# Kernel optimization log

Hardware: AMD Instinct MI355X
Metric: run time of the kernel (lower is better)

Reference implementation:

```python
import jax, jax.numpy as jnp
import numpy as np

NUM_HEADS = 16
WINDOW = 256  # window_size; tokens attend iff |i-j| <= WINDOW//2
LN_EPS = 1e-5


def setup_inputs() -> dict:
    key = jax.random.key(0)
    k1, k2, k3 = jax.random.split(key, 3)
    B, L, D = 2, 2048, 1024
    x = jax.random.normal(k1, (B, L, D), dtype=jnp.float32)
    w_qkv = jax.random.normal(k2, (3 * D, D), dtype=jnp.float32) * 0.02
    w_out = jax.random.normal(k3, (D, D), dtype=jnp.float32) * 0.02
    gamma = jnp.ones((D,), dtype=jnp.float32)
    beta = jnp.zeros((D,), dtype=jnp.float32)
    return {"x": x, "w_qkv": w_qkv, "w_out": w_out, "gamma": gamma, "beta": beta}


def reference(x, w_qkv, w_out, gamma, beta):
    B, L, D = x.shape
    H = NUM_HEADS
    HD = D // H
    residual = x
    # LayerNorm
    mu = jnp.mean(x, axis=-1, keepdims=True)
    var = jnp.mean(jnp.square(x - mu), axis=-1, keepdims=True)
    xn = (x - mu) * jax.lax.rsqrt(var + LN_EPS) * gamma + beta
    # QKV projection (torch Linear: y = x @ W.T)
    qkv = jnp.einsum('bld,ed->ble', xn, w_qkv).reshape(B, L, 3, H, HD)
    qkv = jnp.transpose(qkv, (2, 0, 3, 1, 4))  # [3, B, H, L, HD]
    q, k, v = qkv[0], qkv[1], qkv[2]
    # Dense scores with banded window mask (same math as the torch module)
    scores = jnp.einsum('bhqd,bhkd->bhqk', q, k) / jnp.sqrt(jnp.float32(HD))
    idx = jnp.arange(L)
    band = jnp.abs(idx[:, None] - idx[None, :]) <= (WINDOW // 2)  # [L, L] bool
    scores = jnp.where(band[None, None], scores, -jnp.inf)
    attn = jax.nn.softmax(scores, axis=-1)
    out = jnp.einsum('bhqk,bhkd->bhqd', attn, v)  # [B, H, L, HD]
    out = jnp.transpose(out, (0, 2, 1, 3)).reshape(B, L, D)
    return residual + jnp.einsum('bld,ed->ble', out, w_out)
```

## Files before the change

kernel.cpp:

```cpp
#include <hip/hip_runtime.h>

typedef unsigned int u32;
typedef unsigned short u16;
typedef __attribute__((ext_vector_type(8))) short short8;
typedef __attribute__((ext_vector_type(4))) float f32x4;

#define LSEQ 2048
#define DM 1024
#define HWIN 128
#define QSCALE 0.1803368801111204f

__device__ __forceinline__ u32 pk(float lo, float hi) {
  u32 r;
  asm("v_cvt_pk_bf16_f32 %0, %1, %2" : "=v"(r) : "v"(lo), "v"(hi));
  return r;
}
__device__ __forceinline__ u16 f2bf(float f) {
  union { float f; u32 u; } v; v.f = f;
  u32 r = v.u + 0x7FFFu + ((v.u >> 16) & 1u);
  return (u16)(r >> 16);
}
__device__ __forceinline__ u32 packbf(float lo, float hi) {
  return (u32)f2bf(lo) | ((u32)f2bf(hi) << 16);
}

typedef __attribute__((address_space(3))) u32 lds_u32;
typedef __attribute__((address_space(1))) const u32 glob_u32;
__device__ __forceinline__ void g2lds16(const void* g, void* l) {
  __builtin_amdgcn_global_load_lds((glob_u32*)g, (lds_u32*)l, 16, 0, 0);
}

__global__ __launch_bounds__(256) void ln_cvt_kernel(const float* __restrict__ x,
                                                     const float* __restrict__ gamma,
                                                     const float* __restrict__ beta,
                                                     u16* __restrict__ xn,
                                                     const float* __restrict__ wqi,
                                                     const float* __restrict__ woi,
                                                     u16* __restrict__ wq,
                                                     u16* __restrict__ wo) {
  int blk = blockIdx.x;
  int t = threadIdx.x;
  if (blk >= 4096) {
    const float* in; u16* out; int i;
    if (blk < 7168) { in = wqi; out = wq; i = (blk - 4096) * 256 + t; }
    else            { in = woi; out = wo; i = (blk - 7168) * 256 + t; }
    float4 v = ((const float4*)in)[i];
    u32* dst = (u32*)out + i * 2;
    dst[0] = pk(v.x, v.y);
    dst[1] = pk(v.z, v.w);
    return;
  }
  int r = blk;
  const float4* xr = (const float4*)(x + (size_t)r * DM);
  float4 v = xr[t];
  float s = v.x + v.y + v.z + v.w;
  float s2 = v.x * v.x + v.y * v.y + v.z * v.z + v.w * v.w;
#pragma unroll
  for (int o = 32; o; o >>= 1) { s += __shfl_xor(s, o); s2 += __shfl_xor(s2, o); }
  __shared__ float ws1[4], ws2[4];
  if ((t & 63) == 0) { ws1[t >> 6] = s; ws2[t >> 6] = s2; }
  __syncthreads();
  s = ws1[0] + ws1[1] + ws1[2] + ws1[3];
  s2 = ws2[0] + ws2[1] + ws2[2] + ws2[3];
  float mu = s * (1.0f / DM);
  float var = s2 * (1.0f / DM) - mu * mu;
  float rs = rsqrtf(var + 1e-5f);
  float4 g = ((const float4*)gamma)[t];
  float4 b = ((const float4*)beta)[t];
  u32* dst = (u32*)(xn + (size_t)r * DM) + t * 2;
  dst[0] = pk((v.x - mu) * rs * g.x + b.x, (v.y - mu) * rs * g.y + b.y);
  dst[1] = pk((v.z - mu) * rs * g.z + b.z, (v.w - mu) * rs * g.w + b.w);
}

__device__ __forceinline__ void stage_tile(const u16* __restrict__ G, int gr0, int K,
                                           int k0, u16* lbuf, int tid, int w) {
#pragma unroll
  for (int j = 0; j < 4; ++j) {
    int rp = j * 32 + (tid >> 3);
    int ce = ((tid & 7) ^ (rp & 7)) * 8;
    g2lds16(G + (size_t)(gr0 + rp) * K + k0 + ce, lbuf + j * 2048 + w * 512);
  }
}

template <int MODE>
__global__ __launch_bounds__(256) void gemm_bt(const u16* __restrict__ Ag,
                                               const u16* __restrict__ Bg,
                                               int K, int NB, int NT,
                                               u16* __restrict__ qk_out,
                                               u16* __restrict__ vt_out,
                                               const float* __restrict__ resid,
                                               float* __restrict__ out) {
  __shared__ __align__(16) u16 sm[32768];
  int tid = threadIdx.x;
  int w = tid >> 6, l = tid & 63;
  int lg = l >> 4, li = l & 15;
  int wr = w >> 1, wc = w & 1;

  for (int tile = blockIdx.x; tile < NT; tile += gridDim.x) {
    int bm = tile / NB, bn = tile % NB;
    f32x4 acc[4][4];
#pragma unroll
    for (int m = 0; m < 4; ++m)
#pragma unroll
      for (int n = 0; n < 4; ++n) acc[m][n] = (f32x4){0.f, 0.f, 0.f, 0.f};

    int nt = K >> 6;
    stage_tile(Ag, bm * 128, K, 0, sm, tid, w);
    stage_tile(Bg, bn * 128, K, 0, sm + 8192, tid, w);
    asm volatile("s_waitcnt vmcnt(0)" ::: "memory");
    __builtin_amdgcn_s_barrier();
    asm volatile("" ::: "memory");

    int cur = 0;
    for (int t = 0; t < nt; ++t) {
      if (t + 1 < nt) {
        stage_tile(Ag, bm * 128, K, (t + 1) << 6, sm + (cur ^ 1) * 16384, tid, w);
        stage_tile(Bg, bn * 128, K, (t + 1) << 6, sm + (cur ^ 1) * 16384 + 8192, tid, w);
      }
      const u16* Ab = sm + cur * 16384;
      const u16* Bb = Ab + 8192;
#pragma unroll
      for (int ks = 0; ks < 2; ++ks) {
        short8 af[4], bf4[4];
#pragma unroll
        for (int m = 0; m < 4; ++m)
          af[m] = *(const short8*)&Ab[(wr * 64 + m * 16 + li) * 64 + (((lg + ks * 4) ^ (li & 7)) * 8)];
#pragma unroll
        for (int n = 0; n < 4; ++n)
          bf4[n] = *(const short8*)&Bb[(wc * 64 + n * 16 + li) * 64 + (((lg + ks * 4) ^ (li & 7)) * 8)];
#pragma unroll
        for (int m = 0; m < 4; ++m)
#pragma unroll
          for (int n = 0; n < 4; ++n)
            acc[m][n] = __builtin_amdgcn_mfma_f32_16x16x32_bf16(af[m], bf4[n], acc[m][n], 0, 0, 0);
      }
      asm volatile("s_waitcnt vmcnt(0)" ::: "memory");
      __builtin_amdgcn_s_barrier();
      asm volatile("" ::: "memory");
      cur ^= 1;
    }

    int colbase = bn * 128 + wc * 64;
    int rowbase = bm * 128 + wr * 64;
#pragma unroll
    for (int m = 0; m < 4; ++m) {
      int row = rowbase + m * 16 + lg * 4;
#pragma unroll
      for (int n = 0; n < 4; ++n) {
        int col = colbase + n * 16 + li;
        if (MODE == 0) {
          if (colbase < 2048) {
            float qs = (colbase < 1024) ? QSCALE : 1.0f;
            u32 p01 = pk(acc[m][n][0] * qs, acc[m][n][1] * qs);
            u32 p23 = pk(acc[m][n][2] * qs, acc[m][n][3] * qs);
            qk_out[(size_t)(row + 0) * 2048 + col] = (u16)p01;
            qk_out[(size_t)(row + 1) * 2048 + col] = (u16)(p01 >> 16);
            qk_out[(size_t)(row + 2) * 2048 + col] = (u16)p23;
            qk_out[(size_t)(row + 3) * 2048 + col] = (u16)(p23 >> 16);
          } else {
            int b = row >> 11;
            int hdcol = col - 2048;
            size_t idx = ((size_t)b * 1024 + hdcol) * 2048 + (row & 2047);
            u32* d = (u32*)&vt_out[idx];
            d[0] = pk(acc[m][n][0], acc[m][n][1]);
            d[1] = pk(acc[m][n][2], acc[m][n][3]);
          }
        } else {
#pragma unroll
          for (int r = 0; r < 4; ++r) {
            size_t idx = (size_t)(row + r) * 1024 + col;
            out[idx] = resid[idx] + acc[m][n][r];
          }
        }
      }
    }
  }
}

__global__ __launch_bounds__(256) void attn_kernel(const u16* __restrict__ qk,
                                                   const u16* __restrict__ vt,
                                                   u16* __restrict__ ato) {
  int blk0 = blockIdx.x;
  int xcd = blk0 & 7;
  int j = blk0 >> 3;
  int bh = xcd * 4 + (j & 3);
  int qblk = j >> 2;
  int b = bh >> 4, h = bh & 15;
  int tid = threadIdx.x;
  int w = tid >> 6, l = tid & 63;
  int lg = l >> 4, li = l & 15;
  int qw = qblk * 64 + w * 16;
  int q = qw + li;
  int sg0 = (((2 * lg) & 3) << 4) + li;
  int sg1 = (((2 * lg + 1) & 3) << 4) + li;

  const u16* qbase = qk + (size_t)(b * 2048 + q) * 2048 + h * 64 + lg * 8;
  short8 qf0 = *(const short8*)qbase;
  short8 qf1 = *(const short8*)(qbase + 32);

  const u16* kbase = qk + (size_t)b * 2048 * 2048 + 1024 + h * 64 + lg * 8;
  const u16* vbase = vt + (size_t)(bh * 64 + li) * 2048;

  f32x4 o0 = {0,0,0,0}, o1 = {0,0,0,0}, o2 = {0,0,0,0}, o3 = {0,0,0,0};
  float lsum = 0.f;

  int lo = qw - HWIN; if (lo < 0) lo = 0;
  int hi = qw + 15 + HWIN; if (hi > LSEQ - 1) hi = LSEQ - 1;
  int kb0 = lo & ~31;
  int n = ((hi - kb0) >> 5) + 1;

  for (int c = 0; c < n; ++c) {
    int kb = kb0 + (c << 5);
    const u16* kp0 = kbase + (size_t)(kb + li) * 2048;
    const u16* kp1 = kp0 + (size_t)16 * 2048;
    short8 k00 = *(const short8*)kp0;
    short8 k01 = *(const short8*)(kp0 + 32);
    short8 k10 = *(const short8*)kp1;
    short8 k11 = *(const short8*)(kp1 + 32);
    f32x4 c0 = {0,0,0,0}, c1 = {0,0,0,0};
    c0 = __builtin_amdgcn_mfma_f32_16x16x32_bf16(k00, qf0, c0, 0, 0, 0);
    c0 = __builtin_amdgcn_mfma_f32_16x16x32_bf16(k01, qf1, c0, 0, 0, 0);
    c1 = __builtin_amdgcn_mfma_f32_16x16x32_bf16(k10, qf0, c1, 0, 0, 0);
    c1 = __builtin_amdgcn_mfma_f32_16x16x32_bf16(k11, qf1, c1, 0, 0, 0);

    float p[8];
    bool interior = (kb >= qw + 15 - HWIN) && (kb + 31 <= qw + HWIN);
    if (interior) {
#pragma unroll
      for (int r = 0; r < 4; ++r) {
        p[r]     = __builtin_amdgcn_exp2f(c0[r]);
        p[r + 4] = __builtin_amdgcn_exp2f(c1[r]);
      }
    } else {
      int kd = kb + lg * 4 - q;
#pragma unroll
      for (int r = 0; r < 4; ++r) {
        int d0 = kd + r, d1 = d0 + 16;
        p[r]     = (d0 >= -HWIN && d0 <= HWIN) ? __builtin_amdgcn_exp2f(c0[r]) : 0.f;
        p[r + 4] = (d1 >= -HWIN && d1 <= HWIN) ? __builtin_amdgcn_exp2f(c1[r]) : 0.f;
      }
    }
    lsum += ((p[0] + p[1]) + (p[2] + p[3])) + ((p[4] + p[5]) + (p[6] + p[7]));

    u32 a0 = packbf(p[0], p[1]);
    u32 a1 = packbf(p[2], p[3]);
    u32 b0 = packbf(p[4], p[5]);
    u32 b1 = packbf(p[6], p[7]);
    u32 w0 = (u32)__shfl((int)a0, sg0), w1 = (u32)__shfl((int)a1, sg0);
    u32 w2 = (u32)__shfl((int)a0, sg1), w3 = (u32)__shfl((int)a1, sg1);
    u32 x0 = (u32)__shfl((int)b0, sg0), x1 = (u32)__shfl((int)b1, sg0);
    u32 x2 = (u32)__shfl((int)b0, sg1), x3 = (u32)__shfl((int)b1, sg1);
    bool lohalf = lg < 2;
    union { u32 u[4]; short8 s; } pf;
    pf.u[0] = lohalf ? w0 : x0;
    pf.u[1] = lohalf ? w1 : x1;
    pf.u[2] = lohalf ? w2 : x2;
    pf.u[3] = lohalf ? w3 : x3;

    const u16* vp = vbase + kb + lg * 8;
    short8 v0 = *(const short8*)(vp);
    short8 v1 = *(const short8*)(vp + (size_t)16 * 2048);
    short8 v2 = *(const short8*)(vp + (size_t)32 * 2048);
    short8 v3 = *(const short8*)(vp + (size_t)48 * 2048);
    o0 = __builtin_amdgcn_mfma_f32_16x16x32_bf16(v0, pf.s, o0, 0, 0, 0);
    o1 = __builtin_amdgcn_mfma_f32_16x16x32_bf16(v1, pf.s, o1, 0, 0, 0);
    o2 = __builtin_amdgcn_mfma_f32_16x16x32_bf16(v2, pf.s, o2, 0, 0, 0);
    o3 = __builtin_amdgcn_mfma_f32_16x16x32_bf16(v3, pf.s, o3, 0, 0, 0);
  }

  lsum += __shfl_xor(lsum, 16);
  lsum += __shfl_xor(lsum, 32);
  float inv = 1.0f / lsum;
  u16* orow = ato + (size_t)(b * 2048 + q) * 1024 + h * 64 + lg * 4;
  *(u32*)(orow +  0) = pk(o0[0] * inv, o0[1] * inv);
  *(u32*)(orow +  2) = pk(o0[2] * inv, o0[3] * inv);
  *(u32*)(orow + 16) = pk(o1[0] * inv, o1[1] * inv);
  *(u32*)(orow + 18) = pk(o1[2] * inv, o1[3] * inv);
  *(u32*)(orow + 32) = pk(o2[0] * inv, o2[1] * inv);
  *(u32*)(orow + 34) = pk(o2[2] * inv, o2[3] * inv);
  *(u32*)(orow + 48) = pk(o3[0] * inv, o3[1] * inv);
  *(u32*)(orow + 50) = pk(o3[2] * inv, o3[3] * inv);
}

extern "C" void kernel_launch(void* const* d_in, const int* in_sizes, int n_in,
                              void* d_out, int out_size, void* d_ws, size_t ws_size,
                              hipStream_t stream) {
  const float* x     = (const float*)d_in[0];
  const float* w_qkv = (const float*)d_in[1];
  const float* w_out = (const float*)d_in[2];
  const float* gamma = (const float*)d_in[3];
  const float* beta  = (const float*)d_in[4];
  float* out = (float*)d_out;
  char* ws = (char*)d_ws;

  u16* xn  = (u16*)(ws);
  u16* wq  = (u16*)(ws + 8388608);
  u16* wo  = (u16*)(ws + 14680064);
  u16* qkb = (u16*)(ws + 16777216);
  u16* vt  = (u16*)(ws + 33554432);
  u16* ao  = (u16*)(ws + 41943040);

  ln_cvt_kernel<<<8192, 256, 0, stream>>>(x, gamma, beta, xn, w_qkv, w_out, wq, wo);
  gemm_bt<0><<<512, 256, 0, stream>>>(xn, wq, 1024, 24, 768, qkb, vt, nullptr, nullptr);
  attn_kernel<<<1024, 256, 0, stream>>>(qkb, vt, ao);
  gemm_bt<1><<<256, 256, 0, stream>>>(ao, wo, 1024, 8, 256, nullptr, nullptr, x, out);
}
```

Measured before the change: 104.1 us.

## Share K/V tiles across warps via double-buffered LDS in attention kernel

The attention kernel now stages each 32-key K and V chunk for the whole 64-query block into shared memory, instead of having every warp load K and V directly from global memory. K is loaded asynchronously into an XOR-swizzled buffer, and V goes through registers into a padded buffer. Both are double-buffered so the next chunk is fetched while the current one is computed. This removes redundant global loads across the four warps, at the cost of a block-wide barrier per chunk and a loop that covers the union of the warps' windows, with some warps idling on chunks outside their own window.

Measured after the change: 87.20 us. 1.19x faster.

```diff
diff --git a/kernel.cpp b/kernel.cpp
--- a/kernel.cpp
+++ b/kernel.cpp
@@ -180,16 +180,19 @@
 __global__ __launch_bounds__(256) void attn_kernel(const u16* __restrict__ qk,
                                                    const u16* __restrict__ vt,
                                                    u16* __restrict__ ato) {
+  __shared__ __align__(16) u16 Ks[2][2048];
+  __shared__ __align__(16) u16 Vs[2][64 * 40];
   int blk0 = blockIdx.x;
   int xcd = blk0 & 7;
-  int j = blk0 >> 3;
-  int bh = xcd * 4 + (j & 3);
-  int qblk = j >> 2;
+  int jj = blk0 >> 3;
+  int bh = xcd * 4 + (jj & 3);
+  int qblk = jj >> 2;
   int b = bh >> 4, h = bh & 15;
   int tid = threadIdx.x;
   int w = tid >> 6, l = tid & 63;
   int lg = l >> 4, li = l & 15;
-  int qw = qblk * 64 + w * 16;
+  int qw0 = qblk * 64;
+  int qw = qw0 + w * 16;
   int q = qw + li;
   int sg0 = (((2 * lg) & 3) << 4) + li;
   int sg1 = (((2 * lg + 1) & 3) << 4) + li;
@@ -198,74 +201,98 @@
   short8 qf0 = *(const short8*)qbase;
   short8 qf1 = *(const short8*)(qbase + 32);
 
-  const u16* kbase = qk + (size_t)b * 2048 * 2048 + 1024 + h * 64 + lg * 8;
-  const u16* vbase = vt + (size_t)(bh * 64 + li) * 2048;
-
   f32x4 o0 = {0,0,0,0}, o1 = {0,0,0,0}, o2 = {0,0,0,0}, o3 = {0,0,0,0};
   float lsum = 0.f;
 
-  int lo = qw - HWIN; if (lo < 0) lo = 0;
-  int hi = qw + 15 + HWIN; if (hi > LSEQ - 1) hi = LSEQ - 1;
-  int kb0 = lo & ~31;
-  int n = ((hi - kb0) >> 5) + 1;
-
-  for (int c = 0; c < n; ++c) {
+  int blo = qw0 - HWIN; if (blo < 0) blo = 0;
+  int bhi = qw0 + 63 + HWIN; if (bhi > LSEQ - 1) bhi = LSEQ - 1;
+  int kb0 = blo & ~31;
+  int nc = ((bhi - kb0) >> 5) + 1;
+  int wlo = qw - HWIN, whi = qw + 15 + HWIN;
+
+  int krow = tid >> 3, kcl = tid & 7;
+  const u16* ksrc0 = qk + (size_t)b * 2048 * 2048 + 1024 + h * 64 + ((kcl ^ (krow & 7)) * 8);
+  u16* kdst = &Ks[0][0] + (size_t)tid * 8;
+  int vrow = tid >> 2, vc = tid & 3;
+  const u16* vsrc0 = vt + (size_t)(bh * 64 + vrow) * 2048 + vc * 8;
+
+  g2lds16(ksrc0 + (size_t)(kb0 + krow) * 2048, kdst);
+  short8 vreg = *(const short8*)(vsrc0 + kb0);
+  *(short8*)(&Vs[0][0] + vrow * 40 + vc * 8) = vreg;
+  __syncthreads();
+
+  int cur = 0;
+  for (int c = 0; c < nc; ++c) {
     int kb = kb0 + (c << 5);
-    const u16* kp0 = kbase + (size_t)(kb + li) * 2048;
-    const u16* kp1 = kp0 + (size_t)16 * 2048;
-    short8 k00 = *(const short8*)kp0;
-    short8 k01 = *(const short8*)(kp0 + 32);
-    short8 k10 = *(const short8*)kp1;
-    short8 k11 = *(const short8*)(kp1 + 32);
-    f32x4 c0 = {0,0,0,0}, c1 = {0,0,0,0};
-    c0 = __builtin_amdgcn_mfma_f32_16x16x32_bf16(k00, qf0, c0, 0, 0, 0);
-    c0 = __builtin_amdgcn_mfma_f32_16x16x32_bf16(k01, qf1, c0, 0, 0, 0);
-    c1 = __builtin_amdgcn_mfma_f32_16x16x32_bf16(k10, qf0, c1, 0, 0, 0);
-    c1 = __builtin_amdgcn_mfma_f32_16x16x32_bf16(k11, qf1, c1, 0, 0, 0);
-
-    float p[8];
-    bool interior = (kb >= qw + 15 - HWIN) && (kb + 31 <= qw + HWIN);
-    if (interior) {
-#pragma unroll
-      for (int r = 0; r < 4; ++r) {
-        p[r]     = __builtin_amdgcn_exp2f(c0[r]);
-        p[r + 4] = __builtin_amdgcn_exp2f(c1[r]);
+    if (c + 1 < nc) {
+      g2lds16(ksrc0 + (size_t)(kb + 32 + krow) * 2048, kdst + (cur ^ 1) * 2048);
+      vreg = *(const short8*)(vsrc0 + kb + 32);
+    }
+
+    if (kb + 31 >= wlo && kb <= whi) {
+      const u16* Kb = &Ks[cur][0];
+      const u16* Vb = &Vs[cur][0];
+      int p1 = ((lg ^ (li & 7)) * 8);
+      int p2 = p1 ^ 32;
+      short8 k00 = *(const short8*)&Kb[li * 64 + p1];
+      short8 k01 = *(const short8*)&Kb[li * 64 + p2];
+      short8 k10 = *(const short8*)&Kb[(li + 16) * 64 + p1];
+      short8 k11 = *(const short8*)&Kb[(li + 16) * 64 + p2];
+      f32x4 c0 = {0,0,0,0}, c1 = {0,0,0,0};
+      c0 = __builtin_amdgcn_mfma_f32_16x16x32_bf16(k00, qf0, c0, 0, 0, 0);
+      c0 = __builtin_amdgcn_mfma_f32_16x16x32_bf16(k01, qf1, c0, 0, 0, 0);
+      c1 = __builtin_amdgcn_mfma_f32_16x16x32_bf16(k10, qf0, c1, 0, 0, 0);
+      c1 = __builtin_amdgcn_mfma_f32_16x16x32_bf16(k11, qf1, c1, 0, 0, 0);
+
+      float p[8];
+      bool interior = (kb >= qw + 15 - HWIN) && (kb + 31 <= qw + HWIN);
+      if (interior) {
+#pragma unroll
+        for (int r = 0; r < 4; ++r) {
+          p[r]     = __builtin_amdgcn_exp2f(c0[r]);
+          p[r + 4] = __builtin_amdgcn_exp2f(c1[r]);
+        }
+      } else {
+        int kd = kb + lg * 4 - q;
+#pragma unroll
+        for (int r = 0; r < 4; ++r) {
+          int d0 = kd + r, d1 = d0 + 16;
+          p[r]     = (d0 >= -HWIN && d0 <= HWIN) ? __builtin_amdgcn_exp2f(c0[r]) : 0.f;
+          p[r + 4] = (d1 >= -HWIN && d1 <= HWIN) ? __builtin_amdgcn_exp2f(c1[r]) : 0.f;
+        }
       }
-    } else {
-      int kd = kb + lg * 4 - q;
-#pragma unroll
-      for (int r = 0; r < 4; ++r) {
-        int d0 = kd + r, d1 = d0 + 16;
-        p[r]     = (d0 >= -HWIN && d0 <= HWIN) ? __builtin_amdgcn_exp2f(c0[r]) : 0.f;
-        p[r + 4] = (d1 >= -HWIN && d1 <= HWIN) ? __builtin_amdgcn_exp2f(c1[r]) : 0.f;
-      }
-    }
-    lsum += ((p[0] + p[1]) + (p[2] + p[3])) + ((p[4] + p[5]) + (p[6] + p[7]));
-
-    u32 a0 = packbf(p[0], p[1]);
-    u32 a1 = packbf(p[2], p[3]);
-    u32 b0 = packbf(p[4], p[5]);
-    u32 b1 = packbf(p[6], p[7]);
-    u32 w0 = (u32)__shfl((int)a0, sg0), w1 = (u32)__shfl((int)a1, sg0);
-    u32 w2 = (u32)__shfl((int)a0, sg1), w3 = (u32)__shfl((int)a1, sg1);
-    u32 x0 = (u32)__shfl((int)b0, sg0), x1 = (u32)__shfl((int)b1, sg0);
-    u32 x2 = (u32)__shfl((int)b0, sg1), x3 = (u32)__shfl((int)b1, sg1);
-    bool lohalf = lg < 2;
-    union { u32 u[4]; short8 s; } pf;
-    pf.u[0] = lohalf ? w0 : x0;
-    pf.u[1] = lohalf ? w1 : x1;
-    pf.u[2] = lohalf ? w2 : x2;
-    pf.u[3] = lohalf ? w3 : x3;
-
-    const u16* vp = vbase + kb + lg * 8;
-    short8 v0 = *(const short8*)(vp);
-    short8 v1 = *(const short8*)(vp + (size_t)16 * 2048);
-    short8 v2 = *(const short8*)(vp + (size_t)32 * 2048);
-    short8 v3 = *(const short8*)(vp + (size_t)48 * 2048);
-    o0 = __builtin_amdgcn_mfma_f32_16x16x32_bf16(v0, pf.s, o0, 0, 0, 0);
-    o1 = __builtin_amdgcn_mfma_f32_16x16x32_bf16(v1, pf.s, o1, 0, 0, 0);
-    o2 = __builtin_amdgcn_mfma_f32_16x16x32_bf16(v2, pf.s, o2, 0, 0, 0);
-    o3 = __builtin_amdgcn_mfma_f32_16x16x32_bf16(v3, pf.s, o3, 0, 0, 0);
+      lsum += ((p[0] + p[1]) + (p[2] + p[3])) + ((p[4] + p[5]) + (p[6] + p[7]));
+
+      u32 a0 = packbf(p[0], p[1]);
+      u32 a1 = packbf(p[2], p[3]);
+      u32 b0 = packbf(p[4], p[5]);
+      u32 b1 = packbf(p[6], p[7]);
+      u32 w0 = (u32)__shfl((int)a0, sg0), w1 = (u32)__shfl((int)a1, sg0);
+      u32 w2 = (u32)__shfl((int)a0, sg1), w3 = (u32)__shfl((int)a1, sg1);
+      u32 x0 = (u32)__shfl((int)b0, sg0), x1 = (u32)__shfl((int)b1, sg0);
+      u32 x2 = (u32)__shfl((int)b0, sg1), x3 = (u32)__shfl((int)b1, sg1);
+      bool lohalf = lg < 2;
+      union { u32 u[4]; short8 s; } pf;
+      pf.u[0] = lohalf ? w0 : x0;
+      pf.u[1] = lohalf ? w1 : x1;
+      pf.u[2] = lohalf ? w2 : x2;
+      pf.u[3] = lohalf ? w3 : x3;
+
+      short8 v0 = *(const short8*)&Vb[(li     ) * 40 + lg * 8];
+      short8 v1 = *(const short8*)&Vb[(li + 16) * 40 + lg * 8];
+      short8 v2 = *(const short8*)&Vb[(li + 32) * 40 + lg * 8];
+      short8 v3 = *(const short8*)&Vb[(li + 48) * 40 + lg * 8];
+      o0 = __builtin_amdgcn_mfma_f32_16x16x32_bf16(v0, pf.s, o0, 0, 0, 0);
+      o1 = __builtin_amdgcn_mfma_f32_16x16x32_bf16(v1, pf.s, o1, 0, 0, 0);
+      o2 = __builtin_amdgcn_mfma_f32_16x16x32_bf16(v2, pf.s, o2, 0, 0, 0);
+      o3 = __builtin_amdgcn_mfma_f32_16x16x32_bf16(v3, pf.s, o3, 0, 0, 0);
+    }
+
+    if (c + 1 < nc) {
+      *(short8*)(&Vs[cur ^ 1][0] + vrow * 40 + vc * 8) = vreg;
+    }
+    __syncthreads();
+    cur ^= 1;
   }
 
   lsum += __shfl_xor(lsum, 16);
```
